# Kernel tuning notes

Measured on AMD Instinct MI355X. Metric: run time of the kernel, lower is better.

The kernel has to match this reference:

```python
import jax, jax.numpy as jnp
import numpy as np

UP = 2                # upsample_factor
FILTER_SIZE = 31      # sinc filter kernel size (odd)
CUTOFF = 0.5 / UP     # cutoff frequency (fraction of Nyquist)
LEAKY_SLOPE = 0.01    # torch F.leaky_relu default


def make_sinc_filter(cutoff_freq, filter_size):
    # matches torch: t = linspace(-filter_size//2, filter_size//2, filter_size)
    lo = (-filter_size) // 2  # Python floor division: -31//2 = -16
    hi = filter_size // 2     # 15
    t = jnp.linspace(float(lo), float(hi), filter_size)
    x, y = jnp.meshgrid(t, t, indexing='ij')
    r = jnp.sqrt(x ** 2 + y ** 2) + 1e-10
    f = jnp.sin(2.0 * np.pi * cutoff_freq * r) / (np.pi * r)
    return f / jnp.sum(f)


def _ac_coords(out_n, in_n, dtype):
    # align_corners=True mapping: src = i * (in_n - 1) / (out_n - 1)
    scale = (in_n - 1) / (out_n - 1)
    c = jnp.arange(out_n, dtype=dtype) * jnp.asarray(scale, dtype)
    i0 = jnp.clip(jnp.floor(c).astype(jnp.int32), 0, in_n - 2)
    w = c - i0.astype(dtype)
    return i0, w


def bilinear_ac(x, out_h, out_w):
    # x: [B, C, H, W] -> [B, C, out_h, out_w], bilinear, align_corners=True
    H, W = x.shape[-2], x.shape[-1]
    i0, wy = _ac_coords(out_h, H, x.dtype)
    j0, wx = _ac_coords(out_w, W, x.dtype)
    # rows
    top = x[:, :, i0, :]
    bot = x[:, :, i0 + 1, :]
    xr = top + (bot - top) * wy[:, None]          # [B, C, out_h, W]
    # cols
    left = xr[:, :, :, j0]
    right = xr[:, :, :, j0 + 1]
    return left + (right - left) * wx             # [B, C, out_h, out_w]


def setup_inputs() -> dict:
    key = jax.random.key(0)
    x = jax.random.normal(key, (8, 64, 128, 128), dtype=jnp.float32)
    filt = make_sinc_filter(CUTOFF, FILTER_SIZE).astype(jnp.float32)  # buffer, deterministic
    return {"x": x, "filt": filt}


def reference(x, filt):
    B, C, H, W = x.shape
    k = filt.shape[0]
    up = bilinear_ac(x, H * UP, W * UP)
    # 2) elementwise activation
    act = jax.nn.leaky_relu(up, LEAKY_SLOPE)
    # 3) depthwise sinc low-pass conv, same padding
    kernel = jnp.broadcast_to(filt[None, None], (C, 1, k, k))  # [C,1,k,k]
    filtered = jax.lax.conv_general_dilated(
        act, kernel,
        window_strides=(1, 1),
        padding=[(k // 2, k // 2), (k // 2, k // 2)],
        feature_group_count=C,
        dimension_numbers=('NCHW', 'OIHW', 'NCHW'),
    )
    # 4) bilinear downsample back to original size (align_corners=True)
    return bilinear_ac(filtered, H, W)
```

## Files before the change

kernel.cpp:

```cpp
#include <hip/hip_runtime.h>
#include <hip/hip_bf16.h>

typedef __attribute__((ext_vector_type(8))) short bf16x8;
typedef __attribute__((ext_vector_type(16))) float f32x16;

#define INH   128
#define LEAK  0.01f
#define GSTR  288
#define TSTR  168
#define TROWS 94

__device__ __forceinline__ unsigned short f2bf(float f) {
    __hip_bfloat16 h = __float2bfloat16(f);
    return *(unsigned short*)&h;
}

__device__ __forceinline__ float upsample_one(const float* __restrict__ xc,
                                              int ur, int uc, float UPS) {
    float cr = (float)ur * UPS;
    int r0 = (int)cr; if (r0 > 126) r0 = 126;
    float wr = cr - (float)r0;
    float cs = (float)uc * UPS;
    int s0 = (int)cs; if (s0 > 126) s0 = 126;
    float ws = cs - (float)s0;
    const float* p = xc + r0 * INH + s0;
    float a = p[0], b = p[1], c = p[INH], d = p[INH + 1];
    float top = a + (c - a) * wr;
    float bot = b + (d - b) * wr;
    float val = top + (bot - top) * ws;
    return (val > 0.0f) ? val : (LEAK * val);
}

__global__ void build_table(const float* __restrict__ filt, unsigned short* __restrict__ tab) {
    int idx = blockIdx.x * 256 + threadIdx.x;
    if (idx >= 31 * 4 * 64) return;
    int lane = idx & 63, c = (idx >> 6) & 3, fr = idx >> 8;
    #pragma unroll
    for (int t = 0; t < 8; ++t) {
        int v = 16 * c + 8 * (lane >> 5) + t - (lane & 31);
        float f = (v >= 0 && v <= 30) ? filt[fr * 31 + v] : 0.0f;
        tab[idx * 8 + t] = f2bf(f);
    }
}

__global__ __launch_bounds__(256)
void up_table(const float* __restrict__ x, const float* __restrict__ filt,
              unsigned short* __restrict__ U, unsigned short* __restrict__ tab) {
    const int tid = threadIdx.x;
    if (blockIdx.x < 31) {
        int idx = blockIdx.x * 256 + tid;
        if (idx >= 31 * 4 * 64) return;
        int lane = idx & 63, c = (idx >> 6) & 3, fr = idx >> 8;
        #pragma unroll
        for (int t = 0; t < 8; ++t) {
            int v = 16 * c + 8 * (lane >> 5) + t - (lane & 31);
            float f = (v >= 0 && v <= 30) ? filt[fr * 31 + v] : 0.0f;
            tab[idx * 8 + t] = f2bf(f);
        }
        return;
    }
    const float UPS = (float)(127.0 / 255.0);
    int idx = (blockIdx.x - 31) * 256 + tid;
    int bc = idx / (256 * 72);
    int rem = idx - bc * (256 * 72);
    int r = rem / 72;
    int c4 = (rem - r * 72) * 4;
    const float* __restrict__ xc = x + (size_t)bc * (INH * INH);
    unsigned short o[4];
    #pragma unroll
    for (int e = 0; e < 4; ++e) {
        int uc = c4 + e - 15;
        float val = 0.0f;
        if ((unsigned)uc < 256u) val = upsample_one(xc, r, uc, UPS);
        o[e] = f2bf(val);
    }
    *(uint2*)&U[((size_t)bc * 256 + r) * GSTR + c4] = *(const uint2*)o;
}

__global__ __launch_bounds__(256, 4)
void conv_ds(const unsigned short* __restrict__ U, const unsigned short* __restrict__ tab,
             float* __restrict__ out) {
    __shared__ unsigned short T[TROWS * TSTR];
    const int tid = threadIdx.x;
    const int bx = blockIdx.x;
    const int by = blockIdx.y;
    const int bc = blockIdx.z;
    const float DNS = (float)(255.0 / 127.0);
    const int pr0 = 64 * by;
    const unsigned short* __restrict__ Ub = U + (size_t)bc * 256 * GSTR + bx * 128;

    #pragma unroll
    for (int k = 0; k < 8; ++k) {
        int c = tid + k * 256;
        if (c < TROWS * 20) {
            int row = c / 20;
            int sub = c - row * 20;
            int gr = pr0 + row - 15;
            uint4 v = {0u, 0u, 0u, 0u};
            if ((unsigned)gr < 256u)
                v = *(const uint4*)(Ub + gr * GSTR + sub * 8);
            *(uint4*)&T[row * TSTR + sub * 8] = v;
        }
    }
    __syncthreads();

    const int lane = tid & 63;
    const int w = tid >> 6;
    const int wxs = w & 1;
    const int band = w >> 1;
    const int r32 = lane & 31;
    const int hk = lane >> 5;

    const char* ab = (const char*)T + (32 * band + r32) * (TSTR * 2) + (64 * wxs + 8 * hk) * 2;
    const bf16x8* tv = (const bf16x8*)tab;

    f32x16 acc0 = {0.f,0.f,0.f,0.f,0.f,0.f,0.f,0.f,0.f,0.f,0.f,0.f,0.f,0.f,0.f,0.f};
    f32x16 acc1 = acc0;

    #pragma unroll 2
    for (int fr = 0; fr < 31; ++fr) {
        bf16x8 B0 = tv[(fr * 4 + 0) * 64 + lane];
        bf16x8 B1 = tv[(fr * 4 + 1) * 64 + lane];
        bf16x8 B2 = tv[(fr * 4 + 2) * 64 + lane];
        bf16x8 B3 = tv[(fr * 4 + 3) * 64 + lane];
        const char* u = ab + fr * (TSTR * 2);
        bf16x8 A0 = *(const bf16x8*)(u + 0);
        bf16x8 A1 = *(const bf16x8*)(u + 32);
        bf16x8 A2 = *(const bf16x8*)(u + 64);
        bf16x8 A3 = *(const bf16x8*)(u + 96);
        bf16x8 A4 = *(const bf16x8*)(u + 128);
        bf16x8 A5 = *(const bf16x8*)(u + 160);
        acc0 = __builtin_amdgcn_mfma_f32_32x32x16_bf16(A0, B0, acc0, 0, 0, 0);
        acc1 = __builtin_amdgcn_mfma_f32_32x32x16_bf16(A2, B0, acc1, 0, 0, 0);
        acc0 = __builtin_amdgcn_mfma_f32_32x32x16_bf16(A1, B1, acc0, 0, 0, 0);
        acc1 = __builtin_amdgcn_mfma_f32_32x32x16_bf16(A3, B1, acc1, 0, 0, 0);
        acc0 = __builtin_amdgcn_mfma_f32_32x32x16_bf16(A2, B2, acc0, 0, 0, 0);
        acc1 = __builtin_amdgcn_mfma_f32_32x32x16_bf16(A4, B2, acc1, 0, 0, 0);
        acc0 = __builtin_amdgcn_mfma_f32_32x32x16_bf16(A3, B3, acc0, 0, 0, 0);
        acc1 = __builtin_amdgcn_mfma_f32_32x32x16_bf16(A5, B3, acc1, 0, 0, 0);
    }

    #pragma unroll
    for (int s = 0; s < 2; ++s) {
        int cc = 128 * bx + 64 * wxs + 32 * s + r32;
        const bool doout = (cc & 1) == 0;
        const int oj = cc >> 1;
        const float wxw = (float)oj * DNS - (float)cc;
        #pragma unroll
        for (int p = 0; p < 8; ++p) {
            int rpe = ((p & 1) << 1) + ((p >> 1) << 3) + 4 * hk;
            int cre = 64 * by + 32 * band + rpe;
            int oi = cre >> 1;
            float wyw = (float)oi * DNS - (float)cre;
            float ae, ao;
            if (s == 0) { ae = acc0[2 * p]; ao = acc0[2 * p + 1]; }
            else        { ae = acc1[2 * p]; ao = acc1[2 * p + 1]; }
            float v = ae + (ao - ae) * wyw;
            float vr = __shfl_xor(v, 1, 64);
            if (doout) {
                float o = v + (vr - v) * wxw;
                out[((size_t)bc * 128 + oi) * 128 + oj] = o;
            }
        }
    }
}

#define FUSTR  120
#define FUROWS 158
__global__ __launch_bounds__(256)
void afa_mfma(const float* __restrict__ x, const unsigned short* __restrict__ tab,
              float* __restrict__ out) {
    __shared__ unsigned short Ut[FUROWS * FUSTR];
    const int tid = threadIdx.x;
    const int bx = blockIdx.x, by = blockIdx.y, bc = blockIdx.z;
    const float* __restrict__ xc = x + (size_t)bc * (INH * INH);
    const float UPS = (float)(127.0 / 255.0);
    const float DNS = (float)(255.0 / 127.0);
    const int pr0 = 128 * by, pc0 = 64 * bx;

    for (int idx = tid; idx < FUROWS * (FUSTR / 2); idx += 256) {
        int lr = idx / (FUSTR / 2);
        int lc0 = (idx - lr * (FUSTR / 2)) * 2;
        unsigned pack = 0;
        #pragma unroll
        for (int e = 0; e < 2; ++e) {
            int lc = lc0 + e;
            int ur = pr0 + lr - 15;
            int uc = pc0 + lc - 15;
            float val = 0.0f;
            if (lc < 96 && (unsigned)ur < 256u && (unsigned)uc < 256u)
                val = upsample_one(xc, ur, uc, UPS);
            pack |= (unsigned)f2bf(val) << (16 * e);
        }
        *(unsigned*)&Ut[lr * FUSTR + lc0] = pack;
    }
    __syncthreads();

    const int lane = tid & 63;
    const int w = tid >> 6;
    const int wxs = w & 1, wys = w >> 1;
    const int r32 = lane & 31;
    const int hk = lane >> 5;
    const char* ub = (const char*)Ut + (64 * wys + r32) * (FUSTR * 2) + (32 * wxs + 8 * hk) * 2;
    const bf16x8* tv = (const bf16x8*)tab;
    f32x16 acc0 = {0.f,0.f,0.f,0.f,0.f,0.f,0.f,0.f,0.f,0.f,0.f,0.f,0.f,0.f,0.f,0.f};
    f32x16 acc1 = acc0;

    #pragma unroll 1
    for (int fr = 0; fr < 31; ++fr) {
        bf16x8 B0 = tv[(fr * 4 + 0) * 64 + lane];
        bf16x8 B1 = tv[(fr * 4 + 1) * 64 + lane];
        bf16x8 B2 = tv[(fr * 4 + 2) * 64 + lane];
        bf16x8 B3 = tv[(fr * 4 + 3) * 64 + lane];
        const char* u0 = ub + fr * (FUSTR * 2);
        const char* u1 = u0 + 32 * (FUSTR * 2);
        bf16x8 a;
        a = *(const bf16x8*)(u0 + 0);
        acc0 = __builtin_amdgcn_mfma_f32_32x32x16_bf16(a, B0, acc0, 0, 0, 0);
        a = *(const bf16x8*)(u0 + 32);
        acc0 = __builtin_amdgcn_mfma_f32_32x32x16_bf16(a, B1, acc0, 0, 0, 0);
        a = *(const bf16x8*)(u0 + 64);
        acc0 = __builtin_amdgcn_mfma_f32_32x32x16_bf16(a, B2, acc0, 0, 0, 0);
        a = *(const bf16x8*)(u0 + 96);
        acc0 = __builtin_amdgcn_mfma_f32_32x32x16_bf16(a, B3, acc0, 0, 0, 0);
        a = *(const bf16x8*)(u1 + 0);
        acc1 = __builtin_amdgcn_mfma_f32_32x32x16_bf16(a, B0, acc1, 0, 0, 0);
        a = *(const bf16x8*)(u1 + 32);
        acc1 = __builtin_amdgcn_mfma_f32_32x32x16_bf16(a, B1, acc1, 0, 0, 0);
        a = *(const bf16x8*)(u1 + 64);
        acc1 = __builtin_amdgcn_mfma_f32_32x32x16_bf16(a, B2, acc1, 0, 0, 0);
        a = *(const bf16x8*)(u1 + 96);
        acc1 = __builtin_amdgcn_mfma_f32_32x32x16_bf16(a, B3, acc1, 0, 0, 0);
    }

    const int cc = 64 * bx + 32 * wxs + r32;
    const bool doout = (cc & 1) == 0;
    const int oj = cc >> 1;
    const float wxw = (float)oj * DNS - (float)cc;
    #pragma unroll
    for (int tt = 0; tt < 2; ++tt) {
        int cr0 = 128 * by + 64 * wys + 32 * tt;
        #pragma unroll
        for (int p = 0; p < 8; ++p) {
            int rpe = ((p & 1) << 1) + ((p >> 1) << 3) + 4 * hk;
            int cre = cr0 + rpe;
            int oi = cre >> 1;
            float wyw = (float)oi * DNS - (float)cre;
            float ae, ao;
            if (tt == 0) { ae = acc0[2 * p]; ao = acc0[2 * p + 1]; }
            else         { ae = acc1[2 * p]; ao = acc1[2 * p + 1]; }
            float v = ae + (ao - ae) * wyw;
            float vr = __shfl_xor(v, 1, 64);
            if (doout) {
                float o = v + (vr - v) * wxw;
                out[((size_t)bc * 128 + oi) * 128 + oj] = o;
            }
        }
    }
}

extern "C" void kernel_launch(void* const* d_in, const int* in_sizes, int n_in,
                              void* d_out, int out_size, void* d_ws, size_t ws_size,
                              hipStream_t stream) {
    const float* x    = (const float*)d_in[0];
    const float* filt = (const float*)d_in[1];
    float* out = (float*)d_out;

    unsigned short* tab = (unsigned short*)d_ws;
    const size_t U_OFF  = 131072;
    const size_t U_NEED = U_OFF + (size_t)512 * 256 * GSTR * 2;

    if (ws_size >= U_NEED) {
        unsigned short* U = (unsigned short*)((char*)d_ws + U_OFF);
        up_table<<<31 + 512 * 256 * 72 / 256, 256, 0, stream>>>(x, filt, U, tab);
        dim3 grid(2, 4, 8 * 64);
        conv_ds<<<grid, dim3(256), 0, stream>>>(U, tab, out);
    } else {
        build_table<<<31, 256, 0, stream>>>(filt, tab);
        dim3 grid(4, 2, 8 * 64);
        afa_mfma<<<grid, dim3(256), 0, stream>>>(x, tab, out);
    }
}
```

Measured before the change: 165.6 us.

## Enlarge conv_ds tile to 128x128 with four accumulators per wave

```diff
diff --git a/kernel.cpp b/kernel.cpp
--- a/kernel.cpp
+++ b/kernel.cpp
@@ -7,8 +7,8 @@
 #define INH   128
 #define LEAK  0.01f
 #define GSTR  288
-#define TSTR  168
-#define TROWS 94
+#define TSTR  200
+#define TROWS 158
 
 __device__ __forceinline__ unsigned short f2bf(float f) {
     __hip_bfloat16 h = __float2bfloat16(f);
@@ -77,7 +77,7 @@
     *(uint2*)&U[((size_t)bc * 256 + r) * GSTR + c4] = *(const uint2*)o;
 }
 
-__global__ __launch_bounds__(256, 4)
+__global__ __launch_bounds__(256, 2)
 void conv_ds(const unsigned short* __restrict__ U, const unsigned short* __restrict__ tab,
              float* __restrict__ out) {
     __shared__ unsigned short T[TROWS * TSTR];
@@ -86,16 +86,15 @@
     const int by = blockIdx.y;
     const int bc = blockIdx.z;
     const float DNS = (float)(255.0 / 127.0);
-    const int pr0 = 64 * by;
     const unsigned short* __restrict__ Ub = U + (size_t)bc * 256 * GSTR + bx * 128;
 
     #pragma unroll
-    for (int k = 0; k < 8; ++k) {
+    for (int k = 0; k < 13; ++k) {
         int c = tid + k * 256;
         if (c < TROWS * 20) {
             int row = c / 20;
             int sub = c - row * 20;
-            int gr = pr0 + row - 15;
+            int gr = 128 * by + row - 15;
             uint4 v = {0u, 0u, 0u, 0u};
             if ((unsigned)gr < 256u)
                 v = *(const uint4*)(Ub + gr * GSTR + sub * 8);
@@ -106,55 +105,48 @@
 
     const int lane = tid & 63;
     const int w = tid >> 6;
-    const int wxs = w & 1;
-    const int band = w >> 1;
     const int r32 = lane & 31;
     const int hk = lane >> 5;
 
-    const char* ab = (const char*)T + (32 * band + r32) * (TSTR * 2) + (64 * wxs + 8 * hk) * 2;
+    const char* ab = (const char*)T + (32 * w + r32) * (TSTR * 2) + hk * 16;
     const bf16x8* tv = (const bf16x8*)tab;
 
-    f32x16 acc0 = {0.f,0.f,0.f,0.f,0.f,0.f,0.f,0.f,0.f,0.f,0.f,0.f,0.f,0.f,0.f,0.f};
-    f32x16 acc1 = acc0;
-
-    #pragma unroll 2
+    f32x16 acc[4];
+    #pragma unroll
+    for (int s = 0; s < 4; ++s)
+        acc[s] = (f32x16){0.f,0.f,0.f,0.f,0.f,0.f,0.f,0.f,0.f,0.f,0.f,0.f,0.f,0.f,0.f,0.f};
+
+    #pragma unroll 1
     for (int fr = 0; fr < 31; ++fr) {
-        bf16x8 B0 = tv[(fr * 4 + 0) * 64 + lane];
-        bf16x8 B1 = tv[(fr * 4 + 1) * 64 + lane];
-        bf16x8 B2 = tv[(fr * 4 + 2) * 64 + lane];
-        bf16x8 B3 = tv[(fr * 4 + 3) * 64 + lane];
+        bf16x8 B[4];
+        #pragma unroll
+        for (int km = 0; km < 4; ++km)
+            B[km] = tv[(fr * 4 + km) * 64 + lane];
         const char* u = ab + fr * (TSTR * 2);
-        bf16x8 A0 = *(const bf16x8*)(u + 0);
-        bf16x8 A1 = *(const bf16x8*)(u + 32);
-        bf16x8 A2 = *(const bf16x8*)(u + 64);
-        bf16x8 A3 = *(const bf16x8*)(u + 96);
-        bf16x8 A4 = *(const bf16x8*)(u + 128);
-        bf16x8 A5 = *(const bf16x8*)(u + 160);
-        acc0 = __builtin_amdgcn_mfma_f32_32x32x16_bf16(A0, B0, acc0, 0, 0, 0);
-        acc1 = __builtin_amdgcn_mfma_f32_32x32x16_bf16(A2, B0, acc1, 0, 0, 0);
-        acc0 = __builtin_amdgcn_mfma_f32_32x32x16_bf16(A1, B1, acc0, 0, 0, 0);
-        acc1 = __builtin_amdgcn_mfma_f32_32x32x16_bf16(A3, B1, acc1, 0, 0, 0);
-        acc0 = __builtin_amdgcn_mfma_f32_32x32x16_bf16(A2, B2, acc0, 0, 0, 0);
-        acc1 = __builtin_amdgcn_mfma_f32_32x32x16_bf16(A4, B2, acc1, 0, 0, 0);
-        acc0 = __builtin_amdgcn_mfma_f32_32x32x16_bf16(A3, B3, acc0, 0, 0, 0);
-        acc1 = __builtin_amdgcn_mfma_f32_32x32x16_bf16(A5, B3, acc1, 0, 0, 0);
-    }
-
-    #pragma unroll
-    for (int s = 0; s < 2; ++s) {
-        int cc = 128 * bx + 64 * wxs + 32 * s + r32;
+        bf16x8 A[10];
+        #pragma unroll
+        for (int c = 0; c < 10; ++c)
+            A[c] = *(const bf16x8*)(u + c * 32);
+        #pragma unroll
+        for (int km = 0; km < 4; ++km)
+            #pragma unroll
+            for (int s = 0; s < 4; ++s)
+                acc[s] = __builtin_amdgcn_mfma_f32_32x32x16_bf16(A[2 * s + km], B[km], acc[s], 0, 0, 0);
+    }
+
+    #pragma unroll
+    for (int s = 0; s < 4; ++s) {
+        int cc = 128 * bx + 32 * s + r32;
         const bool doout = (cc & 1) == 0;
         const int oj = cc >> 1;
         const float wxw = (float)oj * DNS - (float)cc;
         #pragma unroll
         for (int p = 0; p < 8; ++p) {
             int rpe = ((p & 1) << 1) + ((p >> 1) << 3) + 4 * hk;
-            int cre = 64 * by + 32 * band + rpe;
+            int cre = 128 * by + 32 * w + rpe;
             int oi = cre >> 1;
             float wyw = (float)oi * DNS - (float)cre;
-            float ae, ao;
-            if (s == 0) { ae = acc0[2 * p]; ao = acc0[2 * p + 1]; }
-            else        { ae = acc1[2 * p]; ao = acc1[2 * p + 1]; }
+            float ae = acc[s][2 * p], ao = acc[s][2 * p + 1];
             float v = ae + (ao - ae) * wyw;
             float vr = __shfl_xor(v, 1, 64);
             if (doout) {
@@ -273,7 +265,7 @@
     if (ws_size >= U_NEED) {
         unsigned short* U = (unsigned short*)((char*)d_ws + U_OFF);
         up_table<<<31 + 512 * 256 * 72 / 256, 256, 0, stream>>>(x, filt, U, tab);
-        dim3 grid(2, 4, 8 * 64);
+        dim3 grid(2, 2, 8 * 64);
         conv_ds<<<grid, dim3(256), 0, stream>>>(U, tab, out);
     } else {
         build_table<<<31, 256, 0, stream>>>(filt, tab);
```

Measured after the change: 171.9 us. +3.8%, slower.
